# Performance work log

Measured on AMD Instinct MI355X. Metric: run time of the kernel, lower is better.

The kernel has to match this reference:

```python
import jax, jax.numpy as jnp
import numpy as np
from jax import lax

B, C, H, W = 16, 256, 64, 64  # inplanes=256, planes=2*inplanes=512


def ste_sign(x):
    # forward: sign(x); backward: clipped straight-through (|x|<=1)
    c = jnp.clip(x, -1.0, 1.0)
    return c + lax.stop_gradient(jnp.sign(x) - c)


def conv_ada(x, w, ka, kw):
    # 1-bit activations scaled by learnable scalar ka
    a_b = ste_sign(x) * ka
    # 1-bit weights with per-out-channel XNOR-style scale * learnable kw
    alpha = jnp.mean(jnp.abs(w), axis=(1, 2, 3), keepdims=True) * kw  # [O,1,1,1]
    w_b = ste_sign(w) * alpha
    return lax.conv_general_dilated(a_b, w_b, window_strides=(1, 1),
                                    padding=((1, 1), (1, 1)),
                                    dimension_numbers=('NCHW', 'OIHW', 'NCHW'))


def prelu(x, slope):
    s = slope.reshape(1, -1, 1, 1)
    return jnp.where(x >= 0, x, s * x)


def pixel_unshuffle2(x):
    b, c, h, w = x.shape
    x = x.reshape(b, c, h // 2, 2, w // 2, 2)
    x = x.transpose(0, 1, 3, 5, 2, 4)  # (b, c, r1, r2, h2, w2)
    return x.reshape(b, c * 4, h // 2, w // 2)


def setup_inputs() -> dict:
    key = jax.random.key(0)
    ks = jax.random.split(key, 8)
    inp = {
        'x': jax.random.normal(ks[0], (B, C, H, W), dtype=jnp.float32),
        'conv1_w': jax.random.normal(ks[1], (C, C, 3, 3), dtype=jnp.float32) * 0.05,
        'conv2_w': jax.random.normal(ks[2], (C // 2, C, 3, 3), dtype=jnp.float32) * 0.05,
        'bias1_': jnp.zeros((1, C, 1, 1), jnp.float32),
        'bias1': jnp.zeros((1, C, 1, 1), jnp.float32),
        'bias2': jnp.zeros((1, C, 1, 1), jnp.float32),
        'bias2_': jnp.zeros((1, C, 1, 1), jnp.float32),
        'bias3': jnp.zeros((1, C // 2, 1, 1), jnp.float32),
        'bias4': jnp.zeros((1, C // 2, 1, 1), jnp.float32),
        'ka1': jnp.asarray(1.0, jnp.float32),
        'kw1': jnp.asarray(0.2, jnp.float32),
        'ka2': jnp.asarray(1.0, jnp.float32),
        'kw2': jnp.asarray(0.2, jnp.float32),
        'prelu1_w': jnp.full((C,), 0.25, jnp.float32),
        'prelu2_w': jnp.full((C // 2,), 0.25, jnp.float32),
    }
    return inp


def reference(x, conv1_w, conv2_w, bias1_, bias1, bias2, bias2_, bias3, bias4,
              ka1, kw1, ka2, kw2, prelu1_w, prelu2_w):
    out = x + bias1_                      # move1_
    out = conv_ada(out, conv1_w, ka1, kw1)  # conv1
    xres = out + x                        # residual add
    # NOTE: in the original forward, move1/prelu1/move2 output is overwritten
    # (dead branch); kept here for faithfulness but it does not affect output.
    _dead = prelu(out + bias1, prelu1_w) + bias2
    out = xres + bias2_                   # move2_
    out = conv_ada(out, conv2_w, ka2, kw2)  # conv2 -> C//2 channels
    shortcut = xres[:, :xres.shape[1] // 2, :, :]
    out = out + shortcut
    out = out + bias3                     # move3
    out = prelu(out, prelu2_w)            # prelu2
    out = out + bias4                     # move4
    out = pixel_unshuffle2(out)           # -> [B, 2*C, H/2, W/2]
    return out
```

## Files before the change

kernel.cpp:

```cpp
#include <hip/hip_runtime.h>
#include <hip/hip_bf16.h>
#include <stdint.h>

#define B_   16
#define C_   256
#define H_   64
#define W_   64
#define PH   66
#define PW   66
#define K1   2304
#define NO1  256
#define NO2  128

typedef unsigned short u16;
typedef signed char i8;
typedef int   int32x4 __attribute__((ext_vector_type(4)));

__device__ __forceinline__ void gl_lds16(const void* src, void* dst) {
    __builtin_amdgcn_global_load_lds(
        (const __attribute__((address_space(1))) unsigned int*)src,
        (__attribute__((address_space(3))) unsigned int*)dst, 16, 0, 0);
}

__device__ __forceinline__ i8 sign_i8(float v) {
    return (v > 0.f) ? (i8)1 : ((v < 0.f) ? (i8)(-1) : (i8)0);
}

__global__ void halo_zero(i8* __restrict__ s1, i8* __restrict__ s2) {
    int t = blockIdx.x * blockDim.x + threadIdx.x;
    const int total = B_ * PH * PW * (C_ / 16);
    if (t >= total) return;
    int pix = t >> 4;
    int c16 = t & 15;
    int pw  = pix % PW;
    int ph  = (pix / PW) % PH;
    if (ph != 0 && ph != PH - 1 && pw != 0 && pw != PW - 1) return;
    int4 z = make_int4(0, 0, 0, 0);
    *(int4*)(s1 + (size_t)pix * C_ + c16 * 16) = z;
    *(int4*)(s2 + (size_t)pix * C_ + c16 * 16) = z;
}

__global__ void prep_s1(const float* __restrict__ x, const float* __restrict__ bias1_,
                        i8* __restrict__ s1) {
    __shared__ i8 tile[64][272];
    int b = blockIdx.x >> 6;
    int h = blockIdx.x & 63;
    int t = threadIdx.x;
    int w  = t & 63;
    int cq = t >> 6;
    for (int i = 0; i < 64; ++i) {
        int c = cq * 64 + i;
        float v = x[((size_t)(b * C_ + c) * H_ + h) * W_ + w] + bias1_[c];
        tile[w][c] = sign_i8(v);
    }
    __syncthreads();
    for (int i = 0; i < 4; ++i) {
        int idx = i * 256 + t;
        int w2  = idx >> 4;
        int cb  = (idx & 15) * 16;
        int4 v = *(const int4*)&tile[w2][cb];
        *(int4*)(s1 + ((size_t)(b * PH + h + 1) * PW + (w2 + 1)) * C_ + cb) = v;
    }
}

__global__ void prep_w(const float* __restrict__ w1, const float* __restrict__ w2,
                       const float* __restrict__ ka1, const float* __restrict__ kw1,
                       const float* __restrict__ ka2, const float* __restrict__ kw2,
                       i8* __restrict__ Bt1, i8* __restrict__ Bt2,
                       float* __restrict__ scale1, float* __restrict__ scale2) {
    int o = blockIdx.x;
    const float* w; i8* Bt; float* scale; float kk;
    if (o < NO1) { w = w1 + (size_t)o * K1;         Bt = Bt1 + (size_t)o * K1;         scale = scale1 + o;         kk = ka1[0] * kw1[0]; }
    else         { int oo = o - NO1;
                   w = w2 + (size_t)oo * K1;        Bt = Bt2 + (size_t)oo * K1;        scale = scale2 + oo;        kk = ka2[0] * kw2[0]; }
    int t = threadIdx.x;
    float s = 0.f;
    for (int e = t; e < K1; e += 256) {
        float v = w[e];
        s += fabsf(v);
        int c = e / 9, tap = e % 9;
        Bt[tap * 256 + c] = sign_i8(v);
    }
    for (int off = 32; off; off >>= 1) s += __shfl_down(s, off);
    __shared__ float red[4];
    if ((t & 63) == 0) red[t >> 6] = s;
    __syncthreads();
    if (t == 0) {
        float tot = red[0] + red[1] + red[2] + red[3];
        *scale = kk * tot * (1.0f / 2304.0f);
    }
}

template<int EPI>
__global__ __launch_bounds__(256)
void gemm_conv(const i8* __restrict__ Sin, const i8* __restrict__ Bt,
               const float* __restrict__ scale,
               const float* __restrict__ xaux,
               const float* __restrict__ biasA,
               const float* __restrict__ bias4,
               const float* __restrict__ slope,
               i8*   __restrict__ s2out,
               float* __restrict__ xres_out,
               float* __restrict__ dout)
{
    __shared__ char lds[32 * 1024];
    char* As = lds;
    char* Bs = lds + 16 * 1024;

    int t  = threadIdx.x;

    int wg    = blockIdx.x;
    int chunk = gridDim.x >> 3;
    int logical = (wg & 7) * chunk + (wg >> 3);
    int nb, mb;
    if (EPI == 1) { nb = logical & 1; mb = logical >> 1; }
    else          { nb = 0;           mb = logical; }
    int b  = mb >> 5;
    int h0 = (mb & 31) * 2;

    int ar  = t >> 3;
    int off = ((t & 7) * 16) ^ (((t >> 3) & 7) << 4);

    int l  = t & 63;
    int wv = t >> 6;
    int wr = wv >> 1;
    int wc = wv & 1;

    int32x4 acc[4][4];
#pragma unroll
    for (int mi = 0; mi < 4; ++mi)
#pragma unroll
        for (int ni = 0; ni < 4; ++ni) acc[mi][ni] = (int32x4){0, 0, 0, 0};

    for (int ks = 0; ks < 18; ++ks) {
        int tap = ks >> 1;
        int c0  = (ks & 1) * 128;
        int dh  = tap / 3, dw = tap % 3;
#pragma unroll
        for (int i = 0; i < 4; ++i) {
            int r  = ar + i * 32;
            int hh = r >> 6, ww = r & 63;
            const i8* ga = Sin + ((size_t)(b * PH + h0 + hh + dh) * PW + (ww + dw)) * C_ + c0 + off;
            gl_lds16(ga, As + r * 128 + ((t & 7) * 16));
        }
#pragma unroll
        for (int i = 0; i < 4; ++i) {
            int r = ar + i * 32;
            int n = nb * 128 + r;
            const i8* gb = Bt + (size_t)n * K1 + tap * 256 + c0 + off;
            gl_lds16(gb, Bs + r * 128 + ((t & 7) * 16));
        }
        __syncthreads();
#pragma unroll
        for (int kk = 0; kk < 2; ++kk) {
            int kb = kk * 64 + ((l >> 4) * 16);
            int rx = (l & 7) << 4;
            int32x4 af[4], bf[4];
#pragma unroll
            for (int mi = 0; mi < 4; ++mi)
                af[mi] = *(const int32x4*)(As + (wr * 64 + mi * 16 + (l & 15)) * 128 + (kb ^ rx));
#pragma unroll
            for (int ni = 0; ni < 4; ++ni)
                bf[ni] = *(const int32x4*)(Bs + (wc * 64 + ni * 16 + (l & 15)) * 128 + (kb ^ rx));
#pragma unroll
            for (int mi = 0; mi < 4; ++mi)
#pragma unroll
                for (int ni = 0; ni < 4; ++ni)
                    acc[mi][ni] = __builtin_amdgcn_mfma_i32_16x16x64_i8(af[mi], bf[ni], acc[mi][ni], 0, 0, 0);
        }
        __syncthreads();
    }

    int co = l & 15;
    int ro = l >> 4;
#pragma unroll
    for (int mi = 0; mi < 4; ++mi) {
#pragma unroll
        for (int ni = 0; ni < 4; ++ni) {
            int n_loc = wc * 64 + ni * 16 + co;
            int o = nb * 128 + n_loc;
            float sc = scale[o];
#pragma unroll
            for (int j = 0; j < 4; ++j) {
                int m_loc = wr * 64 + mi * 16 + ro * 4 + j;
                int h = h0 + (m_loc >> 6);
                int w = m_loc & 63;
                float v = (float)acc[mi][ni][j] * sc;
                if (EPI == 1) {
                    float xv = xaux[((size_t)(b * C_ + o) * H_ + h) * W_ + w];
                    float xr = v + xv;
                    float sv = xr + biasA[o];
                    s2out[((size_t)(b * PH + h + 1) * PW + (w + 1)) * C_ + o] = sign_i8(sv);
                    if (o < NO2)
                        xres_out[(((size_t)b * H_ + h) * W_ + w) * NO2 + o] = xr;
                } else {
                    float xr = xaux[(((size_t)b * H_ + h) * W_ + w) * NO2 + o];
                    float vv = v + xr + biasA[o];
                    vv = (vv >= 0.f) ? vv : vv * slope[o];
                    vv += bias4[o];
                    int p = h & 1, q = w & 1;
                    dout[(((size_t)b * 512 + (o * 4 + p * 2 + q)) * 32 + (h >> 1)) * 32 + (w >> 1)] = vv;
                }
            }
        }
    }
}

static const size_t SZ_S   = (size_t)B_ * PH * PW * C_;
static const size_t OFF_S1 = 0;
static const size_t OFF_S2 = OFF_S1 + SZ_S;
static const size_t OFF_B1 = OFF_S2 + SZ_S;
static const size_t OFF_B2 = OFF_B1 + (size_t)NO1 * K1;
static const size_t OFF_C1 = OFF_B2 + (size_t)NO2 * K1;
static const size_t OFF_C2 = OFF_C1 + 1024;
static const size_t OFF_XR = OFF_C2 + 512;

extern "C" void kernel_launch(void* const* d_in, const int* in_sizes, int n_in,
                              void* d_out, int out_size, void* d_ws, size_t ws_size,
                              hipStream_t stream) {
    (void)in_sizes; (void)n_in; (void)out_size; (void)ws_size;
    const float* x      = (const float*)d_in[0];
    const float* w1     = (const float*)d_in[1];
    const float* w2     = (const float*)d_in[2];
    const float* bias1_ = (const float*)d_in[3];
    const float* bias2_ = (const float*)d_in[6];
    const float* bias3  = (const float*)d_in[7];
    const float* bias4  = (const float*)d_in[8];
    const float* ka1    = (const float*)d_in[9];
    const float* kw1    = (const float*)d_in[10];
    const float* ka2    = (const float*)d_in[11];
    const float* kw2    = (const float*)d_in[12];
    const float* slope2 = (const float*)d_in[14];

    char* ws = (char*)d_ws;
    i8*    s1   = (i8*)(ws + OFF_S1);
    i8*    s2   = (i8*)(ws + OFF_S2);
    i8*    Bt1  = (i8*)(ws + OFF_B1);
    i8*    Bt2  = (i8*)(ws + OFF_B2);
    float* sc1  = (float*)(ws + OFF_C1);
    float* sc2  = (float*)(ws + OFF_C2);
    float* xres = (float*)(ws + OFF_XR);
    float* out  = (float*)d_out;

    {
        int total = B_ * PH * PW * (C_ / 16);
        hipLaunchKernelGGL(halo_zero, dim3((total + 255) / 256), dim3(256), 0, stream, s1, s2);
    }
    hipLaunchKernelGGL(prep_s1, dim3(B_ * H_), dim3(256), 0, stream, x, bias1_, s1);
    hipLaunchKernelGGL(prep_w, dim3(NO1 + NO2), dim3(256), 0, stream,
                       w1, w2, ka1, kw1, ka2, kw2, Bt1, Bt2, sc1, sc2);
    hipLaunchKernelGGL((gemm_conv<1>), dim3(1024), dim3(256), 0, stream,
                       s1, Bt1, sc1, x, bias2_, nullptr, nullptr, s2, xres, nullptr);
    hipLaunchKernelGGL((gemm_conv<2>), dim3(512), dim3(256), 0, stream,
                       s2, Bt2, sc2, xres, bias3, bias4, slope2, nullptr, nullptr, out);
}
```

Baseline: 278.3 us.

## Triple-buffer LDS pipeline with larger 256x128 tiles and 512-thread blocks

Replaces the single-buffered load/sync/compute loop of the int8 MFMA conv GEMM with a three-stage LDS ring. Loads are issued two k-steps ahead, and partial vmcnt waits plus raw barriers hide global-to-LDS latency behind MFMA work. The M tile doubles to four image rows (256 pixels) with 8 waves per block, which halves the grid and reuses each B tile across more rows. It also raises wave priority around the MFMA section. The cost is 144KB of dynamic LDS per block, which forces one block per CU and may need an attribute to allow that much dynamic shared memory.

```diff
diff --git a/kernel.cpp b/kernel.cpp
--- a/kernel.cpp
+++ b/kernel.cpp
@@ -12,7 +12,6 @@
 #define NO1  256
 #define NO2  128
 
-typedef unsigned short u16;
 typedef signed char i8;
 typedef int   int32x4 __attribute__((ext_vector_type(4)));
 
@@ -92,7 +91,7 @@
 }
 
 template<int EPI>
-__global__ __launch_bounds__(256)
+__global__ __launch_bounds__(512)
 void gemm_conv(const i8* __restrict__ Sin, const i8* __restrict__ Bt,
                const float* __restrict__ scale,
                const float* __restrict__ xaux,
@@ -103,9 +102,7 @@
                float* __restrict__ xres_out,
                float* __restrict__ dout)
 {
-    __shared__ char lds[32 * 1024];
-    char* As = lds;
-    char* Bs = lds + 16 * 1024;
+    extern __shared__ char lds[];
 
     int t  = threadIdx.x;
 
@@ -115,11 +112,12 @@
     int nb, mb;
     if (EPI == 1) { nb = logical & 1; mb = logical >> 1; }
     else          { nb = 0;           mb = logical; }
-    int b  = mb >> 5;
-    int h0 = (mb & 31) * 2;
-
-    int ar  = t >> 3;
+    int b  = mb >> 4;
+    int h0 = (mb & 15) * 4;
+
+    int r0  = t >> 3;
     int off = ((t & 7) * 16) ^ (((t >> 3) & 7) << 4);
+    int lin = (t & 7) * 16;
 
     int l  = t & 63;
     int wv = t >> 6;
@@ -132,25 +130,32 @@
 #pragma unroll
         for (int ni = 0; ni < 4; ++ni) acc[mi][ni] = (int32x4){0, 0, 0, 0};
 
-    for (int ks = 0; ks < 18; ++ks) {
+    auto stage = [&](int ks, char* buf) {
+        char* As = buf;
+        char* Bs = buf + 32768;
         int tap = ks >> 1;
         int c0  = (ks & 1) * 128;
         int dh  = tap / 3, dw = tap % 3;
 #pragma unroll
         for (int i = 0; i < 4; ++i) {
-            int r  = ar + i * 32;
+            int r  = r0 + i * 64;
             int hh = r >> 6, ww = r & 63;
             const i8* ga = Sin + ((size_t)(b * PH + h0 + hh + dh) * PW + (ww + dw)) * C_ + c0 + off;
-            gl_lds16(ga, As + r * 128 + ((t & 7) * 16));
-        }
-#pragma unroll
-        for (int i = 0; i < 4; ++i) {
-            int r = ar + i * 32;
+            gl_lds16(ga, As + r * 128 + lin);
+        }
+#pragma unroll
+        for (int i = 0; i < 2; ++i) {
+            int r = r0 + i * 64;
             int n = nb * 128 + r;
             const i8* gb = Bt + (size_t)n * K1 + tap * 256 + c0 + off;
-            gl_lds16(gb, Bs + r * 128 + ((t & 7) * 16));
-        }
-        __syncthreads();
+            gl_lds16(gb, Bs + r * 128 + lin);
+        }
+    };
+
+    auto compute = [&](const char* buf) {
+        const char* As = buf;
+        const char* Bs = buf + 32768;
+        __builtin_amdgcn_s_setprio(1);
 #pragma unroll
         for (int kk = 0; kk < 2; ++kk) {
             int kb = kk * 64 + ((l >> 4) * 16);
@@ -168,7 +173,25 @@
                 for (int ni = 0; ni < 4; ++ni)
                     acc[mi][ni] = __builtin_amdgcn_mfma_i32_16x16x64_i8(af[mi], bf[ni], acc[mi][ni], 0, 0, 0);
         }
-        __syncthreads();
+        __builtin_amdgcn_s_setprio(0);
+    };
+
+    char* bc  = lds;
+    char* bn  = lds + 49152;
+    char* bn2 = lds + 98304;
+
+    stage(0, bc);
+    stage(1, bn);
+    asm volatile("s_waitcnt vmcnt(6)" ::: "memory");
+    __builtin_amdgcn_s_barrier();
+
+    for (int ks = 0; ks < 18; ++ks) {
+        if (ks < 16) stage(ks + 2, bn2);
+        compute(bc);
+        if (ks < 16)      asm volatile("s_waitcnt vmcnt(6)" ::: "memory");
+        else if (ks == 16) asm volatile("s_waitcnt vmcnt(0)" ::: "memory");
+        if (ks < 17) __builtin_amdgcn_s_barrier();
+        char* tmp = bc; bc = bn; bn = bn2; bn2 = tmp;
     }
 
     int co = l & 15;
@@ -249,8 +272,8 @@
     hipLaunchKernelGGL(prep_s1, dim3(B_ * H_), dim3(256), 0, stream, x, bias1_, s1);
     hipLaunchKernelGGL(prep_w, dim3(NO1 + NO2), dim3(256), 0, stream,
                        w1, w2, ka1, kw1, ka2, kw2, Bt1, Bt2, sc1, sc2);
-    hipLaunchKernelGGL((gemm_conv<1>), dim3(1024), dim3(256), 0, stream,
+    hipLaunchKernelGGL((gemm_conv<1>), dim3(512), dim3(512), 147456, stream,
                        s1, Bt1, sc1, x, bias2_, nullptr, nullptr, s2, xres, nullptr);
-    hipLaunchKernelGGL((gemm_conv<2>), dim3(512), dim3(256), 0, stream,
+    hipLaunchKernelGGL((gemm_conv<2>), dim3(256), dim3(512), 147456, stream,
                        s2, Bt2, sc2, xres, bias3, bias4, slope2, nullptr, nullptr, out);
 }
```

Result: faster. 267.6 us (-3.8%).
